# Kernel optimization log

Measured on AMD Instinct MI355X. Metric: run time of the kernel, lower is better.

## Reference

```python
import jax, jax.numpy as jnp
import numpy as np

N_NODES = 100000
N_EDGES = 800000
DIM = 64
HEADS = 4
HEAD_DIM = DIM // HEADS  # 16
ALPHA = 0.1
K_ITERS = 8  # fixed-point iterations approximating the implicit/CG solve


def setup_inputs() -> dict:
    key = jax.random.key(0)
    ks = jax.random.split(key, 7)
    x = jax.random.normal(ks[0], (N_NODES, DIM), dtype=jnp.float32)
    edge_index = jax.random.randint(ks[1], (2, N_EDGES), 0, N_NODES, dtype=jnp.int64)
    edge_attr = jax.random.normal(ks[2], (N_EDGES, DIM), dtype=jnp.float32)
    s = 1.0 / np.sqrt(DIM)
    Wq = jax.random.normal(ks[3], (DIM, DIM), dtype=jnp.float32) * s
    Wk = jax.random.normal(ks[4], (DIM, DIM), dtype=jnp.float32) * s
    Wv = jax.random.normal(ks[5], (DIM, DIM), dtype=jnp.float32) * s
    We = jax.random.normal(ks[6], (DIM, DIM), dtype=jnp.float32) * s
    return {"x": x, "edge_index": edge_index, "edge_attr": edge_attr,
            "Wq": Wq, "Wk": Wk, "Wv": Wv, "We": We}


def _mapr(x, edge_index, edge_attr, Wq, Wk, Wv, We):
    N = x.shape[0]
    src, dst = edge_index[0], edge_index[1]
    q = (x @ Wq).reshape(N, HEADS, HEAD_DIM)
    k = (x @ Wk).reshape(N, HEADS, HEAD_DIM)
    v = (x @ Wv).reshape(N, HEADS, HEAD_DIM)
    e = (edge_attr @ We).reshape(-1, HEADS, HEAD_DIM)
    # per-edge multi-head dot attention logits, edge features modulate keys
    logits = jnp.sum(q[dst] * (k[src] + e), axis=-1) / np.sqrt(HEAD_DIM)  # [E,H]
    # segment softmax over incoming edges of each dst node
    m = jax.ops.segment_max(logits, dst, num_segments=N)  # [N,H]
    ex = jnp.exp(logits - m[dst])
    denom = jax.ops.segment_sum(ex, dst, num_segments=N)  # [N,H]
    att = ex / (denom[dst] + 1e-16)  # [E,H]
    # implicit propagation: fixed-point solve of z = alpha*v + (1-alpha) * A_att z
    def step(z, _):
        msg = att[:, :, None] * z[src]                       # [E,H,D]
        agg = jax.ops.segment_sum(msg, dst, num_segments=N)  # [N,H,D]
        return ALPHA * v + (1.0 - ALPHA) * agg, None
    z, _ = jax.lax.scan(step, v, None, length=K_ITERS)
    return z.reshape(N, DIM)


def reference(x, edge_index, edge_attr, Wq, Wk, Wv, We):
    h = _mapr(x, edge_index, edge_attr, Wq, Wk, Wv, We)
    h = jax.nn.relu(h)  # act; dropout is identity in eval mode
    return x + h        # residual
```

## Files before the change

### kernel.cpp

```cpp
#include <hip/hip_runtime.h>
#include <hip/hip_fp16.h>
#include <cstdint>
#include <cstddef>

#define NN 100000
#define NE 800000
#define DIM 64
#define HEADS 4
#define HEAD_DIM 16
#define ALPHA 0.1f
#define K_ITERS 8
#define NBLK 391

typedef short bf16x8 __attribute__((ext_vector_type(8)));
typedef float f32x4 __attribute__((ext_vector_type(4)));

__device__ __forceinline__ unsigned short f2bf(float f) {
    unsigned int x = __float_as_uint(f);
    unsigned int r = (x + 0x7fffu + ((x >> 16) & 1u)) >> 16;
    return (unsigned short)r;
}
__device__ __forceinline__ float bf_lo(unsigned int p) { return __uint_as_float(p << 16); }
__device__ __forceinline__ float bf_hi(unsigned int p) { return __uint_as_float(p & 0xffff0000u); }

__device__ __forceinline__ float2 h2f(unsigned int v) {
    __half2 h = *(__half2*)&v;
    return __half22float2(h);
}
__device__ __forceinline__ unsigned int f2h2(float a, float b) {
    __half2 h = __floats2half2_rn(a, b);
    return *(unsigned int*)&h;
}
__device__ __forceinline__ float dot8h(uint4 a, uint4 b) {
    float2 a0 = h2f(a.x), b0 = h2f(b.x);
    float2 a1 = h2f(a.y), b1 = h2f(b.y);
    float2 a2 = h2f(a.z), b2 = h2f(b.z);
    float2 a3 = h2f(a.w), b3 = h2f(b.w);
    return a0.x * b0.x + a0.y * b0.y + a1.x * b1.x + a1.y * b1.y
         + a2.x * b2.x + a2.y * b2.y + a3.x * b3.x + a3.y * b3.y;
}

#define ACC8(a, V) { float2 t_; \
    t_ = h2f((V).x); m[0] += (a) * t_.x; m[1] += (a) * t_.y; \
    t_ = h2f((V).y); m[2] += (a) * t_.x; m[3] += (a) * t_.y; \
    t_ = h2f((V).z); m[4] += (a) * t_.x; m[5] += (a) * t_.y; \
    t_ = h2f((V).w); m[6] += (a) * t_.x; m[7] += (a) * t_.y; }

__global__ __launch_bounds__(256) void qkv_mfma_kernel(
    const float* __restrict__ x,
    const float* __restrict__ Wq, const float* __restrict__ Wk,
    const float* __restrict__ Wv, const float* __restrict__ We,
    __half* __restrict__ qh, __half* __restrict__ kh, __half* __restrict__ vh,
    unsigned short* __restrict__ u)
{
    __shared__ unsigned short sq[64 * 72];
    int tid = threadIdx.x;
    int w = tid >> 6;
    int lane = tid & 63;
    int m16 = lane & 15;
    int quad = lane >> 4;
    int node = blockIdx.x * 64 + w * 16 + m16;
    int nodeC = node < NN ? node : NN - 1;

    bf16x8 afrag[2];
    #pragma unroll
    for (int kk = 0; kk < 2; ++kk) {
        const float* xr = x + (size_t)nodeC * DIM + kk * 32 + quad * 8;
        #pragma unroll
        for (int j = 0; j < 8; ++j) afrag[kk][j] = (short)f2bf(xr[j]);
    }

    const float* Ws[3] = {Wq, Wk, Wv};
    __half* outs[3] = {qh, kh, vh};

    #pragma unroll
    for (int mtx = 0; mtx < 3; ++mtx) {
        const float* W = Ws[mtx];
        #pragma unroll
        for (int n0 = 0; n0 < 64; n0 += 16) {
            int col = n0 + m16;
            f32x4 acc = {0.f, 0.f, 0.f, 0.f};
            #pragma unroll
            for (int kk = 0; kk < 2; ++kk) {
                bf16x8 bfrag;
                #pragma unroll
                for (int j = 0; j < 8; ++j)
                    bfrag[j] = (short)f2bf(W[(kk * 32 + quad * 8 + j) * DIM + col]);
                acc = __builtin_amdgcn_mfma_f32_16x16x32_bf16(afrag[kk], bfrag, acc, 0, 0, 0);
            }
            if (mtx == 0) {
                #pragma unroll
                for (int r = 0; r < 4; ++r) acc[r] *= 0.25f;
            }
            #pragma unroll
            for (int r = 0; r < 4; ++r) {
                int rl = w * 16 + quad * 4 + r;
                int gnode = blockIdx.x * 64 + rl;
                if (mtx == 0) sq[rl * 72 + col] = f2bf(acc[r]);
                if (gnode < NN) outs[mtx][(size_t)gnode * DIM + col] = __float2half(acc[r]);
            }
        }
    }
    __syncthreads();

    #pragma unroll
    for (int h = 0; h < HEADS; ++h) {
        int kk = h >> 1;
        bf16x8 aq;
        const unsigned short* sr = &sq[(w * 16 + m16) * 72 + kk * 32 + quad * 8];
        #pragma unroll
        for (int j = 0; j < 8; ++j) aq[j] = (short)sr[j];
        #pragma unroll
        for (int c0 = 0; c0 < 64; c0 += 16) {
            int c = c0 + m16;
            bf16x8 bfrag;
            #pragma unroll
            for (int j = 0; j < 8; ++j) {
                int k = kk * 32 + quad * 8 + j;
                bfrag[j] = ((k >> 4) == h) ? (short)f2bf(We[c * DIM + k]) : (short)0;
            }
            f32x4 acc = {0.f, 0.f, 0.f, 0.f};
            acc = __builtin_amdgcn_mfma_f32_16x16x32_bf16(aq, bfrag, acc, 0, 0, 0);
            #pragma unroll
            for (int r = 0; r < 4; ++r) {
                int gnode = blockIdx.x * 64 + w * 16 + quad * 4 + r;
                if (gnode < NN) u[(size_t)gnode * 256 + h * 64 + c] = f2bf(acc[r]);
            }
        }
    }
}

__global__ void init_kernel(float* __restrict__ denom, int* __restrict__ deg) {
    int i = blockIdx.x * 256 + threadIdx.x;
    if (i < NN * HEADS) denom[i] = 0.f;
    if (i < NN) deg[i] = 0;
}

__global__ void deg_kernel(const int* __restrict__ ei, int* __restrict__ deg) {
    int e = blockIdx.x * 256 + threadIdx.x;
    if (e >= NE) return;
    atomicAdd(&deg[ei[NE + e]], 1);
}

__global__ void blocksum_kernel(const int* __restrict__ deg, int* __restrict__ bsum) {
    int t = threadIdx.x, b = blockIdx.x;
    int idx = b * 256 + t;
    int v = (idx < NN) ? deg[idx] : 0;
    #pragma unroll
    for (int off = 32; off > 0; off >>= 1) v += __shfl_down(v, off);
    __shared__ int wsum[4];
    if ((t & 63) == 0) wsum[t >> 6] = v;
    __syncthreads();
    if (t == 0) bsum[b] = wsum[0] + wsum[1] + wsum[2] + wsum[3];
}

__global__ void bscan_kernel(const int* __restrict__ bsum, int* __restrict__ boff) {
    __shared__ int s[512];
    int t = threadIdx.x;
    int v = (t < NBLK) ? bsum[t] : 0;
    s[t] = v;
    __syncthreads();
    for (int off = 1; off < 512; off <<= 1) {
        int u = (t >= off) ? s[t - off] : 0;
        __syncthreads();
        s[t] += u;
        __syncthreads();
    }
    if (t < NBLK) boff[t] = s[t] - v;
}

__global__ void rowptr_kernel(const int* __restrict__ deg, const int* __restrict__ boff,
                              int* __restrict__ row_ptr, int* __restrict__ cursor) {
    __shared__ int s[256];
    int t = threadIdx.x, b = blockIdx.x;
    int idx = b * 256 + t;
    int v = (idx < NN) ? deg[idx] : 0;
    s[t] = v;
    __syncthreads();
    for (int off = 1; off < 256; off <<= 1) {
        int u = (t >= off) ? s[t - off] : 0;
        __syncthreads();
        s[t] += u;
        __syncthreads();
    }
    if (idx < NN) {
        int ex = boff[b] + s[t] - v;
        row_ptr[idx] = ex;
        cursor[idx] = ex;
    }
    if (idx == 0) row_ptr[NN] = NE;
}

__global__ void scatter_kernel(const int* __restrict__ ei,
                               int* __restrict__ cursor,
                               int* __restrict__ csr_src,
                               int* __restrict__ csr_e,
                               int* __restrict__ csr_dst) {
    int e = blockIdx.x * 256 + threadIdx.x;
    if (e >= NE) return;
    int src = ei[e], dst = ei[NE + e];
    int pos = atomicAdd(&cursor[dst], 1);
    csr_src[pos] = src;
    csr_e[pos] = e;
    csr_dst[pos] = dst;
}

__global__ void logits_csr_kernel(const __half* __restrict__ qh,
                                  const __half* __restrict__ kh,
                                  const float* __restrict__ edge_attr,
                                  const unsigned short* __restrict__ u,
                                  const int* __restrict__ csr_src,
                                  const int* __restrict__ csr_e,
                                  const int* __restrict__ csr_dst,
                                  __half* __restrict__ att,
                                  float* __restrict__ denom) {
    int idx = blockIdx.x * 256 + threadIdx.x;
    if (idx >= NE * HEADS) return;
    int j = idx >> 2, h = idx & 3;
    int src = csr_src[j], dst = csr_dst[j], e = csr_e[j];
    const float4* attr4 = (const float4*)edge_attr + (size_t)e * 16;
    const uint4* u4 = (const uint4*)u + (size_t)dst * 32 + h * 8;
    float au = 0.f;
    #pragma unroll
    for (int i = 0; i < 8; ++i) {
        uint4 up = u4[i];
        float4 a0 = attr4[2 * i];
        float4 a1 = attr4[2 * i + 1];
        au += a0.x * bf_lo(up.x) + a0.y * bf_hi(up.x)
            + a0.z * bf_lo(up.y) + a0.w * bf_hi(up.y)
            + a1.x * bf_lo(up.z) + a1.y * bf_hi(up.z)
            + a1.z * bf_lo(up.w) + a1.w * bf_hi(up.w);
    }
    const uint4* qq = (const uint4*)qh + (size_t)dst * 8 + h * 2;
    const uint4* kk = (const uint4*)kh + (size_t)src * 8 + h * 2;
    float qk = dot8h(qq[0], kk[0]) + dot8h(qq[1], kk[1]);
    float ex = __expf(qk + au);
    att[idx] = __float2half(ex);
    atomicAdd(&denom[dst * HEADS + h], ex);
}

__global__ void prop_csr_kernel(const __half* __restrict__ zin,
                                const __half* __restrict__ vh,
                                const __half* __restrict__ att,
                                const int* __restrict__ csr_src,
                                const int* __restrict__ row_ptr,
                                const float* __restrict__ denom,
                                __half* __restrict__ zout) {
    int gid = blockIdx.x * 256 + threadIdx.x;
    int node = gid >> 3;
    if (node >= NN) return;
    int l = gid & 7;
    int head = l >> 1;
    const uint4* z4 = (const uint4*)zin;
    float m[8];
    #pragma unroll
    for (int i = 0; i < 8; ++i) m[i] = 0.f;
    int beg = row_ptr[node], end = row_ptr[node + 1];
    int j = beg;
    for (; j + 4 <= end; j += 4) {
        int s0 = csr_src[j], s1 = csr_src[j + 1], s2 = csr_src[j + 2], s3 = csr_src[j + 3];
        float a0 = __half2float(att[4 * j + head]);
        float a1 = __half2float(att[4 * j + 4 + head]);
        float a2 = __half2float(att[4 * j + 8 + head]);
        float a3 = __half2float(att[4 * j + 12 + head]);
        uint4 z0 = z4[(size_t)s0 * 8 + l];
        uint4 z1 = z4[(size_t)s1 * 8 + l];
        uint4 z2 = z4[(size_t)s2 * 8 + l];
        uint4 z3 = z4[(size_t)s3 * 8 + l];
        ACC8(a0, z0); ACC8(a1, z1); ACC8(a2, z2); ACC8(a3, z3);
    }
    for (; j < end; ++j) {
        int s = csr_src[j];
        float a = __half2float(att[4 * j + head]);
        uint4 zl = z4[(size_t)s * 8 + l];
        ACC8(a, zl);
    }
    float r = 0.9f / (denom[node * HEADS + head] + 1e-16f);
    uint4 vv = ((const uint4*)vh)[(size_t)node * 8 + l];
    float2 v0 = h2f(vv.x), v1 = h2f(vv.y), v2 = h2f(vv.z), v3 = h2f(vv.w);
    uint4 o;
    o.x = f2h2(ALPHA * v0.x + r * m[0], ALPHA * v0.y + r * m[1]);
    o.y = f2h2(ALPHA * v1.x + r * m[2], ALPHA * v1.y + r * m[3]);
    o.z = f2h2(ALPHA * v2.x + r * m[4], ALPHA * v2.y + r * m[5]);
    o.w = f2h2(ALPHA * v3.x + r * m[6], ALPHA * v3.y + r * m[7]);
    ((uint4*)zout)[(size_t)node * 8 + l] = o;
}

__global__ void prop_out_kernel(const __half* __restrict__ zin,
                                const __half* __restrict__ vh,
                                const __half* __restrict__ att,
                                const int* __restrict__ csr_src,
                                const int* __restrict__ row_ptr,
                                const float* __restrict__ denom,
                                const float* __restrict__ x,
                                float* __restrict__ out) {
    int gid = blockIdx.x * 256 + threadIdx.x;
    int node = gid >> 3;
    if (node >= NN) return;
    int l = gid & 7;
    int head = l >> 1;
    const uint4* z4 = (const uint4*)zin;
    float m[8];
    #pragma unroll
    for (int i = 0; i < 8; ++i) m[i] = 0.f;
    int beg = row_ptr[node], end = row_ptr[node + 1];
    int j = beg;
    for (; j + 4 <= end; j += 4) {
        int s0 = csr_src[j], s1 = csr_src[j + 1], s2 = csr_src[j + 2], s3 = csr_src[j + 3];
        float a0 = __half2float(att[4 * j + head]);
        float a1 = __half2float(att[4 * j + 4 + head]);
        float a2 = __half2float(att[4 * j + 8 + head]);
        float a3 = __half2float(att[4 * j + 12 + head]);
        uint4 z0 = z4[(size_t)s0 * 8 + l];
        uint4 z1 = z4[(size_t)s1 * 8 + l];
        uint4 z2 = z4[(size_t)s2 * 8 + l];
        uint4 z3 = z4[(size_t)s3 * 8 + l];
        ACC8(a0, z0); ACC8(a1, z1); ACC8(a2, z2); ACC8(a3, z3);
    }
    for (; j < end; ++j) {
        int s = csr_src[j];
        float a = __half2float(att[4 * j + head]);
        uint4 zl = z4[(size_t)s * 8 + l];
        ACC8(a, zl);
    }
    float r = 0.9f / (denom[node * HEADS + head] + 1e-16f);
    uint4 vv = ((const uint4*)vh)[(size_t)node * 8 + l];
    float2 v0 = h2f(vv.x), v1 = h2f(vv.y), v2 = h2f(vv.z), v3 = h2f(vv.w);
    float zf[8] = { ALPHA * v0.x + r * m[0], ALPHA * v0.y + r * m[1],
                    ALPHA * v1.x + r * m[2], ALPHA * v1.y + r * m[3],
                    ALPHA * v2.x + r * m[4], ALPHA * v2.y + r * m[5],
                    ALPHA * v3.x + r * m[6], ALPHA * v3.y + r * m[7] };
    const float4* x4 = (const float4*)x + (size_t)node * 16 + l * 2;
    float4 xa = x4[0], xb = x4[1];
    float4 oa, ob;
    oa.x = xa.x + fmaxf(zf[0], 0.f); oa.y = xa.y + fmaxf(zf[1], 0.f);
    oa.z = xa.z + fmaxf(zf[2], 0.f); oa.w = xa.w + fmaxf(zf[3], 0.f);
    ob.x = xb.x + fmaxf(zf[4], 0.f); ob.y = xb.y + fmaxf(zf[5], 0.f);
    ob.z = xb.z + fmaxf(zf[6], 0.f); ob.w = xb.w + fmaxf(zf[7], 0.f);
    float4* o4 = (float4*)out + (size_t)node * 16 + l * 2;
    o4[0] = oa; o4[1] = ob;
}

extern "C" void kernel_launch(void* const* d_in, const int* in_sizes, int n_in,
                              void* d_out, int out_size, void* d_ws, size_t ws_size,
                              hipStream_t stream) {
    const float* x         = (const float*)d_in[0];
    const int*   ei        = (const int*)d_in[1];
    const float* edge_attr = (const float*)d_in[2];
    const float* Wq        = (const float*)d_in[3];
    const float* Wk        = (const float*)d_in[4];
    const float* Wv        = (const float*)d_in[5];
    const float* We        = (const float*)d_in[6];
    float* out = (float*)d_out;

    __half* qh = (__half*)d_ws;
    __half* kh = qh + (size_t)NN * DIM;
    __half* vh = kh + (size_t)NN * DIM;
    unsigned short* u = (unsigned short*)(vh + (size_t)NN * DIM);
    __half* zha = (__half*)(u + (size_t)NN * 256);
    __half* zhb = zha + (size_t)NN * DIM;
    __half* att = zhb + (size_t)NN * DIM;
    float* denom = (float*)(att + (size_t)NE * HEADS);
    int* deg     = (int*)(denom + (size_t)NN * HEADS);
    int* bsum    = deg + NN;
    int* boff    = bsum + NBLK;
    int* row_ptr = boff + NBLK;
    int* cursor  = row_ptr + NN + 1;
    int* csr_src = cursor + NN;
    int* csr_e   = csr_src + NE;
    int* csr_dst = csr_e + NE;

    hipLaunchKernelGGL(qkv_mfma_kernel, dim3((NN + 63) / 64), dim3(256), 0, stream,
                       x, Wq, Wk, Wv, We, qh, kh, vh, u);
    hipLaunchKernelGGL(init_kernel, dim3((NN * HEADS + 255) / 256), dim3(256), 0, stream,
                       denom, deg);
    hipLaunchKernelGGL(deg_kernel, dim3((NE + 255) / 256), dim3(256), 0, stream,
                       ei, deg);
    hipLaunchKernelGGL(blocksum_kernel, dim3(NBLK), dim3(256), 0, stream,
                       deg, bsum);
    hipLaunchKernelGGL(bscan_kernel, dim3(1), dim3(512), 0, stream,
                       bsum, boff);
    hipLaunchKernelGGL(rowptr_kernel, dim3(NBLK), dim3(256), 0, stream,
                       deg, boff, row_ptr, cursor);
    hipLaunchKernelGGL(scatter_kernel, dim3((NE + 255) / 256), dim3(256), 0, stream,
                       ei, cursor, csr_src, csr_e, csr_dst);
    hipLaunchKernelGGL(logits_csr_kernel, dim3(NE * HEADS / 256), dim3(256), 0, stream,
                       qh, kh, edge_attr, u, csr_src, csr_e, csr_dst, att, denom);

    const __half* zin = vh;
    __half* zout = zha;
    for (int it = 0; it < K_ITERS - 1; ++it) {
        hipLaunchKernelGGL(prop_csr_kernel, dim3((NN * 8 + 255) / 256), dim3(256), 0, stream,
                           zin, vh, att, csr_src, row_ptr, denom, zout);
        zin = zout;
        zout = (zout == zha) ? zhb : zha;
    }
    hipLaunchKernelGGL(prop_out_kernel, dim3((NN * 8 + 255) / 256), dim3(256), 0, stream,
                       zin, vh, att, csr_src, row_ptr, denom, x, out);
}
```

Before: 735.5 us.

## Sort nodes by degree for propagation and coalesce edge-attr loads in logits

Adds a degree histogram, scan and permutation so the propagation kernels process nodes grouped by in-degree. This is meant to reduce wave divergence from uneven neighbour loops. The logits kernel is also restructured so 16 lanes cooperatively load one edge's attribute row with coalesced float4 reads and reduce the four head dot products via shuffles. In exchange it adds three small launches, an extra indirection per node in every propagation pass, and scattered output writes.

```diff
diff --git a/kernel.cpp b/kernel.cpp
--- a/kernel.cpp
+++ b/kernel.cpp
@@ -11,6 +11,7 @@
 #define ALPHA 0.1f
 #define K_ITERS 8
 #define NBLK 391
+#define MAXD 64
 
 typedef short bf16x8 __attribute__((ext_vector_type(8)));
 typedef float f32x4 __attribute__((ext_vector_type(4)));
@@ -38,6 +39,9 @@
     float2 a3 = h2f(a.w), b3 = h2f(b.w);
     return a0.x * b0.x + a0.y * b0.y + a1.x * b1.x + a1.y * b1.y
          + a2.x * b2.x + a2.y * b2.y + a3.x * b3.x + a3.y * b3.y;
+}
+__device__ __forceinline__ float dot4bf(float4 a, uint2 p) {
+    return a.x * bf_lo(p.x) + a.y * bf_hi(p.x) + a.z * bf_lo(p.y) + a.w * bf_hi(p.y);
 }
 
 #define ACC8(a, V) { float2 t_; \
@@ -130,10 +134,12 @@
     }
 }
 
-__global__ void init_kernel(float* __restrict__ denom, int* __restrict__ deg) {
+__global__ void init_kernel(float* __restrict__ denom, int* __restrict__ deg,
+                            int* __restrict__ hist) {
     int i = blockIdx.x * 256 + threadIdx.x;
     if (i < NN * HEADS) denom[i] = 0.f;
     if (i < NN) deg[i] = 0;
+    if (i < MAXD) hist[i] = 0;
 }
 
 __global__ void deg_kernel(const int* __restrict__ ei, int* __restrict__ deg) {
@@ -189,6 +195,37 @@
         cursor[idx] = ex;
     }
     if (idx == 0) row_ptr[NN] = NE;
+}
+
+__global__ void dhist_kernel(const int* __restrict__ deg, int* __restrict__ hist) {
+    __shared__ int lh[MAXD];
+    int t = threadIdx.x;
+    if (t < MAXD) lh[t] = 0;
+    __syncthreads();
+    int i = blockIdx.x * 256 + t;
+    if (i < NN) atomicAdd(&lh[min(deg[i], MAXD - 1)], 1);
+    __syncthreads();
+    if (t < MAXD && lh[t]) atomicAdd(&hist[t], lh[t]);
+}
+
+__global__ void dscan_kernel(const int* __restrict__ hist, int* __restrict__ dcur) {
+    int l = threadIdx.x;
+    int v = hist[l];
+    int s = v;
+    #pragma unroll
+    for (int off = 1; off < 64; off <<= 1) {
+        int o = __shfl_up(s, off);
+        if (l >= off) s += o;
+    }
+    dcur[l] = s - v;
+}
+
+__global__ void dperm_kernel(const int* __restrict__ deg, int* __restrict__ dcur,
+                             int* __restrict__ perm) {
+    int i = blockIdx.x * 256 + threadIdx.x;
+    if (i >= NN) return;
+    int pos = atomicAdd(&dcur[min(deg[i], MAXD - 1)], 1);
+    perm[pos] = i;
 }
 
 __global__ void scatter_kernel(const int* __restrict__ ei,
@@ -214,29 +251,40 @@
                                   const int* __restrict__ csr_dst,
                                   __half* __restrict__ att,
                                   float* __restrict__ denom) {
-    int idx = blockIdx.x * 256 + threadIdx.x;
-    if (idx >= NE * HEADS) return;
-    int j = idx >> 2, h = idx & 3;
-    int src = csr_src[j], dst = csr_dst[j], e = csr_e[j];
-    const float4* attr4 = (const float4*)edge_attr + (size_t)e * 16;
-    const uint4* u4 = (const uint4*)u + (size_t)dst * 32 + h * 8;
-    float au = 0.f;
-    #pragma unroll
-    for (int i = 0; i < 8; ++i) {
-        uint4 up = u4[i];
-        float4 a0 = attr4[2 * i];
-        float4 a1 = attr4[2 * i + 1];
-        au += a0.x * bf_lo(up.x) + a0.y * bf_hi(up.x)
-            + a0.z * bf_lo(up.y) + a0.w * bf_hi(up.y)
-            + a1.x * bf_lo(up.z) + a1.y * bf_hi(up.z)
-            + a1.z * bf_lo(up.w) + a1.w * bf_hi(up.w);
-    }
-    const uint4* qq = (const uint4*)qh + (size_t)dst * 8 + h * 2;
-    const uint4* kk = (const uint4*)kh + (size_t)src * 8 + h * 2;
-    float qk = dot8h(qq[0], kk[0]) + dot8h(qq[1], kk[1]);
-    float ex = __expf(qk + au);
-    att[idx] = __float2half(ex);
-    atomicAdd(&denom[dst * HEADS + h], ex);
+    int wave = threadIdx.x >> 6;
+    int lane = threadIdx.x & 63;
+    int r = lane >> 4, c = lane & 15;
+    int jbase = blockIdx.x * 64 + wave * 16;
+    #pragma unroll
+    for (int g = 0; g < 4; ++g) {
+        int j = jbase + g * 4 + r;
+        int e = csr_e[j], dst = csr_dst[j];
+        float4 a4 = ((const float4*)edge_attr)[(size_t)e * 16 + c];
+        const uint2* ub = (const uint2*)(u + (size_t)dst * 256);
+        float4 au;
+        au.x = dot4bf(a4, ub[0 * 16 + c]);
+        au.y = dot4bf(a4, ub[1 * 16 + c]);
+        au.z = dot4bf(a4, ub[2 * 16 + c]);
+        au.w = dot4bf(a4, ub[3 * 16 + c]);
+        #pragma unroll
+        for (int msk = 8; msk >= 1; msk >>= 1) {
+            au.x += __shfl_xor(au.x, msk);
+            au.y += __shfl_xor(au.y, msk);
+            au.z += __shfl_xor(au.z, msk);
+            au.w += __shfl_xor(au.w, msk);
+        }
+        if (c < 4) {
+            int h = c;
+            float auh = (h == 0) ? au.x : (h == 1) ? au.y : (h == 2) ? au.z : au.w;
+            int src = csr_src[j];
+            const uint4* qq = (const uint4*)qh + (size_t)dst * 8 + h * 2;
+            const uint4* kk = (const uint4*)kh + (size_t)src * 8 + h * 2;
+            float qk = dot8h(qq[0], kk[0]) + dot8h(qq[1], kk[1]);
+            float ex = __expf(qk + auh);
+            att[4 * j + h] = __float2half(ex);
+            atomicAdd(&denom[dst * HEADS + h], ex);
+        }
+    }
 }
 
 __global__ void prop_csr_kernel(const __half* __restrict__ zin,
@@ -245,10 +293,12 @@
                                 const int* __restrict__ csr_src,
                                 const int* __restrict__ row_ptr,
                                 const float* __restrict__ denom,
+                                const int* __restrict__ perm,
                                 __half* __restrict__ zout) {
     int gid = blockIdx.x * 256 + threadIdx.x;
-    int node = gid >> 3;
-    if (node >= NN) return;
+    int nidx = gid >> 3;
+    if (nidx >= NN) return;
+    int node = perm[nidx];
     int l = gid & 7;
     int head = l >> 1;
     const uint4* z4 = (const uint4*)zin;
@@ -292,11 +342,13 @@
                                 const int* __restrict__ csr_src,
                                 const int* __restrict__ row_ptr,
                                 const float* __restrict__ denom,
+                                const int* __restrict__ perm,
                                 const float* __restrict__ x,
                                 float* __restrict__ out) {
     int gid = blockIdx.x * 256 + threadIdx.x;
-    int node = gid >> 3;
-    if (node >= NN) return;
+    int nidx = gid >> 3;
+    if (nidx >= NN) return;
+    int node = perm[nidx];
     int l = gid & 7;
     int head = l >> 1;
     const uint4* z4 = (const uint4*)zin;
@@ -369,11 +421,14 @@
     int* csr_src = cursor + NN;
     int* csr_e   = csr_src + NE;
     int* csr_dst = csr_e + NE;
+    int* hist    = csr_dst + NE;
+    int* dcur    = hist + MAXD;
+    int* perm    = dcur + MAXD;
 
     hipLaunchKernelGGL(qkv_mfma_kernel, dim3((NN + 63) / 64), dim3(256), 0, stream,
                        x, Wq, Wk, Wv, We, qh, kh, vh, u);
     hipLaunchKernelGGL(init_kernel, dim3((NN * HEADS + 255) / 256), dim3(256), 0, stream,
-                       denom, deg);
+                       denom, deg, hist);
     hipLaunchKernelGGL(deg_kernel, dim3((NE + 255) / 256), dim3(256), 0, stream,
                        ei, deg);
     hipLaunchKernelGGL(blocksum_kernel, dim3(NBLK), dim3(256), 0, stream,
@@ -382,19 +437,25 @@
                        bsum, boff);
     hipLaunchKernelGGL(rowptr_kernel, dim3(NBLK), dim3(256), 0, stream,
                        deg, boff, row_ptr, cursor);
+    hipLaunchKernelGGL(dhist_kernel, dim3(NBLK), dim3(256), 0, stream,
+                       deg, hist);
+    hipLaunchKernelGGL(dscan_kernel, dim3(1), dim3(64), 0, stream,
+                       hist, dcur);
+    hipLaunchKernelGGL(dperm_kernel, dim3(NBLK), dim3(256), 0, stream,
+                       deg, dcur, perm);
     hipLaunchKernelGGL(scatter_kernel, dim3((NE + 255) / 256), dim3(256), 0, stream,
                        ei, cursor, csr_src, csr_e, csr_dst);
-    hipLaunchKernelGGL(logits_csr_kernel, dim3(NE * HEADS / 256), dim3(256), 0, stream,
+    hipLaunchKernelGGL(logits_csr_kernel, dim3(NE / 64), dim3(256), 0, stream,
                        qh, kh, edge_attr, u, csr_src, csr_e, csr_dst, att, denom);
 
     const __half* zin = vh;
     __half* zout = zha;
     for (int it = 0; it < K_ITERS - 1; ++it) {
         hipLaunchKernelGGL(prop_csr_kernel, dim3((NN * 8 + 255) / 256), dim3(256), 0, stream,
-                           zin, vh, att, csr_src, row_ptr, denom, zout);
+                           zin, vh, att, csr_src, row_ptr, denom, perm, zout);
         zin = zout;
         zout = (zout == zha) ? zhb : zha;
     }
     hipLaunchKernelGGL(prop_out_kernel, dim3((NN * 8 + 255) / 256), dim3(256), 0, stream,
-                       zin, vh, att, csr_src, row_ptr, denom, x, out);
-}
+                       zin, vh, att, csr_src, row_ptr, denom, perm, x, out);
+}
```

New measurement: 1.105 ms. 1.5x slower.
